# Optimization experiments

Measured on AMD Instinct MI355X. Metric: run time of the kernel, lower is better.

Reference implementation:

```python
import math
import jax, jax.numpy as jnp
import numpy as np

FIRE_THRESH = 0.85
_C = math.sqrt(2.0 / math.pi)

def _normalize(v, axis=-1, eps=1e-12):
    # matches torch F.normalize: v / max(||v||, eps)
    n = jnp.linalg.norm(v, axis=axis, keepdims=True)
    return v / jnp.maximum(n, eps)

def setup_inputs() -> dict:
    key = jax.random.key(0)
    k1, k2, k3 = jax.random.split(key, 3)
    B, T, D, N = 8, 4096, 1024, 512
    x = jax.random.normal(k1, (B, T, D), dtype=jnp.float32)
    buf = jax.random.normal(k2, (N, D), dtype=jnp.float32)
    depl = jax.random.uniform(k3, (N,), dtype=jnp.float32)
    mask = jnp.ones((N,), dtype=bool)
    ptr = 3  # static ring-buffer write position
    log_k = jnp.asarray(math.log(2.0), dtype=jnp.float32)
    logit_depl_rate = jnp.asarray(0.0, dtype=jnp.float32)
    logit_floor = jnp.asarray(math.log(0.1 / 0.9), dtype=jnp.float32)
    return {"x": x, "buf": buf, "depl": depl, "mask": mask, "ptr": ptr,
            "log_k": log_k, "logit_depl_rate": logit_depl_rate, "logit_floor": logit_floor}

def reference(x, buf, depl, mask, ptr, log_k, logit_depl_rate, logit_floor):
    # steady-state (_ready=True) forward of GELU244
    k_gate = jnp.clip(jnp.exp(log_k), 0.1, 8.0)
    depl_rate = 0.1 + 0.8 * jax.nn.sigmoid(logit_depl_rate)
    floor_val = 0.5 * jax.nn.sigmoid(logit_floor)
    # tanh-approx GELU
    y = 0.5 * x * (1.0 + jnp.tanh(_C * (x + 0.044715 * x ** 3)))  # [B,T,D]
    D = x.shape[-1]
    m_curr = jax.lax.stop_gradient(jnp.mean(y.reshape(-1, D), axis=0))  # [D]
    m_n = _normalize(m_curr, axis=0)  # unit vector [D]
    buf_n = _normalize(buf, axis=-1)  # [N,D]
    sims = jnp.where(mask, buf_n @ m_n, -1.0)  # [N]
    idx = jnp.argmax(sims)
    max_sim = sims[idx]
    depl_level = depl[idx]
    # .item() in torch => no grad through k_gate / depl_level here
    raw_gate = jnp.exp(-jax.lax.stop_gradient(k_gate) * (1.0 - jax.lax.stop_gradient(depl_level)))
    gate = floor_val + (1.0 - floor_val) * raw_gate
    output = y * gate
    # no_grad state update: deplete fired slot, write m_n at ring pointer
    factor = jnp.where(max_sim > FIRE_THRESH, jax.lax.stop_gradient(depl_rate), 1.0)
    new_depl = depl.at[idx].multiply(factor)
    new_buf = buf.at[ptr].set(m_n)
    new_depl = new_depl.at[ptr].set(1.0)
    new_mask = mask.at[ptr].set(True)
    return output, new_buf, new_depl, new_mask
```

## Files before the change

### kernel.cpp

```cpp
#include <hip/hip_runtime.h>
#include <math.h>

#define D_DIM    1024
#define D4       256
#define A_BLOCKS 1024
#define N_SLOTS  512
#define OUT_GRID 2048

#define GK1 0.07135481627f
#define GK2 1.59576912161f

typedef float f32x4 __attribute__((ext_vector_type(4)));

__device__ __forceinline__ float gelu_tanh(float x) {
    float t = x * __builtin_fmaf(GK1, x * x, GK2);
    float e = __expf(-t);
    return x * __builtin_amdgcn_rcpf(1.0f + e);
}

__global__ __launch_bounds__(256) void colsum_partial(
        const float* __restrict__ x, const float* __restrict__ buf,
        float* __restrict__ partial, float* __restrict__ out_buf,
        const int* __restrict__ ptr_p, int rows, int rows_per_block) {
    int t = threadIdx.x;
    int b = blockIdx.x;
    if (b < N_SLOTS && b != ptr_p[0])
        ((float4*)(out_buf + (size_t)b * D_DIM))[t] =
            ((const float4*)(buf + (size_t)b * D_DIM))[t];
    const float4* x4 = (const float4*)x;
    float4 acc = make_float4(0.f, 0.f, 0.f, 0.f);
    int r0 = b * rows_per_block;
    #pragma unroll 8
    for (int r = r0; r < r0 + rows_per_block; ++r) {
        float4 v = x4[(size_t)r * D4 + t];
        acc.x += gelu_tanh(v.x);
        acc.y += gelu_tanh(v.y);
        acc.z += gelu_tanh(v.z);
        acc.w += gelu_tanh(v.w);
    }
    ((float4*)partial)[(size_t)b * D4 + t] = acc;
}

__global__ __launch_bounds__(256) void reduce_cols(
        const float* __restrict__ partial, float* __restrict__ s_out) {
    __shared__ float red[8][32];
    int t  = threadIdx.x, b = blockIdx.x;
    int cl = t & 31, sl = t >> 5;
    int c  = b * 32 + cl;
    float s = 0.f;
    int p0 = sl * (A_BLOCKS / 8);
    #pragma unroll 4
    for (int p = p0; p < p0 + A_BLOCKS / 8; ++p)
        s += partial[(size_t)p * D_DIM + c];
    red[sl][cl] = s;
    __syncthreads();
    if (t < 32) {
        float tot = 0.f;
        #pragma unroll
        for (int i = 0; i < 8; ++i) tot += red[i][t];
        s_out[b * 32 + t] = tot;
    }
}

__global__ __launch_bounds__(256) void sims_dot(
        const float* __restrict__ buf, const float* __restrict__ s_vec,
        float* __restrict__ dotraw) {
    int n = blockIdx.x, t = threadIdx.x;
    int wid = t >> 6, lane = t & 63;
    float4 v = ((const float4*)(buf + (size_t)n * D_DIM))[t];
    float4 w = ((const float4*)s_vec)[t];
    float dot = v.x*w.x + v.y*w.y + v.z*w.z + v.w*w.w;
    float sq  = v.x*v.x + v.y*v.y + v.z*v.z + v.w*v.w;
    #pragma unroll
    for (int off = 32; off > 0; off >>= 1) {
        dot += __shfl_down(dot, off, 64);
        sq  += __shfl_down(sq,  off, 64);
    }
    __shared__ float rd[4], rs[4];
    if (lane == 0) { rd[wid] = dot; rs[wid] = sq; }
    __syncthreads();
    if (t == 0)
        dotraw[n] = (rd[0] + rd[1] + rd[2] + rd[3]) /
                    fmaxf(sqrtf(rs[0] + rs[1] + rs[2] + rs[3]), 1e-12f);
}

__global__ __launch_bounds__(256) void gate_stream_out(
        const float* __restrict__ x, const float* __restrict__ dotraw,
        const float* __restrict__ s_vec, const float* __restrict__ depl,
        const float* __restrict__ log_k, const float* __restrict__ logit_depl_rate,
        const float* __restrict__ logit_floor, const int* __restrict__ ptr_p,
        float* __restrict__ out, float* __restrict__ out_buf,
        float* __restrict__ out_depl, float* __restrict__ out_mask,
        int n4, float eps_s) {
    __shared__ float sval[256];
    __shared__ int   sidx[256];
    __shared__ float sgate;
    int t = threadIdx.x, b = blockIdx.x;

    {
        float a  = dotraw[t];
        float b2 = dotraw[t + 256];
        float v; int id;
        if (b2 > a) { v = b2; id = t + 256; } else { v = a; id = t; }
        sval[t] = v; sidx[t] = id;
        __syncthreads();
        for (int s = 128; s > 0; s >>= 1) {
            if (t < s) {
                float av = sval[t], bv = sval[t + s];
                int   ai = sidx[t], bi = sidx[t + s];
                if (bv > av || (bv == av && bi < ai)) { sval[t] = bv; sidx[t] = bi; }
            }
            __syncthreads();
        }
        if (t == 0) {
            int idx = sidx[0];
            float k_gate    = fminf(fmaxf(__expf(log_k[0]), 0.1f), 8.0f);
            float floor_val = 0.5f / (1.0f + __expf(-logit_floor[0]));
            float raw_gate  = __expf(-k_gate * (1.0f - depl[idx]));
            sgate = floor_val + (1.0f - floor_val) * raw_gate;
        }
        __syncthreads();
    }

    if (b == 0) {
        float4 w0 = ((const float4*)s_vec)[t];
        float sq = w0.x*w0.x + w0.y*w0.y + w0.z*w0.z + w0.w*w0.w;
        #pragma unroll
        for (int off = 32; off > 0; off >>= 1) sq += __shfl_down(sq, off, 64);
        __shared__ float rs2[4];
        __shared__ float ssnorm;
        int wid = t >> 6, lane = t & 63;
        if (lane == 0) rs2[wid] = sq;
        __syncthreads();
        if (t == 0)
            ssnorm = fmaxf(sqrtf(rs2[0] + rs2[1] + rs2[2] + rs2[3]), eps_s);
        __syncthreads();
        float snorm = ssnorm;
        int idx = sidx[0];
        int ptr = ptr_p[0];
        float max_sim   = sval[0] / snorm;
        float depl_rate = 0.1f + 0.8f / (1.0f + __expf(-logit_depl_rate[0]));
        float fac = (max_sim > 0.85f) ? depl_rate : 1.0f;
        #pragma unroll
        for (int j = t; j < N_SLOTS; j += 256) {
            float nd = depl[j] * (j == idx ? fac : 1.0f);
            if (j == ptr) nd = 1.0f;
            out_depl[j] = nd;
            out_mask[j] = 1.0f;
        }
        float inv = 1.0f / snorm;
        float4 sv = ((const float4*)s_vec)[t];
        float4 mn = make_float4(sv.x*inv, sv.y*inv, sv.z*inv, sv.w*inv);
        ((float4*)(out_buf + (size_t)ptr * D_DIM))[t] = mn;
    }

    float gate = sgate;
    const f32x4* x4 = (const f32x4*)x;
    f32x4* o4 = (f32x4*)out;
    #pragma unroll 4
    for (int i = b * 256 + t; i < n4; i += OUT_GRID * 256) {
        f32x4 v = x4[i];
        f32x4 r;
        r.x = gelu_tanh(v.x) * gate;
        r.y = gelu_tanh(v.y) * gate;
        r.z = gelu_tanh(v.z) * gate;
        r.w = gelu_tanh(v.w) * gate;
        __builtin_nontemporal_store(r, o4 + i);
    }
}

extern "C" void kernel_launch(void* const* d_in, const int* in_sizes, int n_in,
                              void* d_out, int out_size, void* d_ws, size_t ws_size,
                              hipStream_t stream) {
    const float* x     = (const float*)d_in[0];
    const float* buf   = (const float*)d_in[1];
    const float* depl  = (const float*)d_in[2];
    const int*   ptr_p = (const int*)d_in[4];
    const float* log_k = (const float*)d_in[5];
    const float* ldr   = (const float*)d_in[6];
    const float* lf    = (const float*)d_in[7];

    int xN   = in_sizes[0];
    int bufN = in_sizes[1];
    int rows = xN / D_DIM;

    float* out      = (float*)d_out;
    float* out_buf  = out + xN;
    float* out_depl = out_buf + bufN;
    float* out_mask = out_depl + N_SLOTS;

    float* ws      = (float*)d_ws;
    float* s_vec   = ws;
    float* dotraw  = ws + 1040;
    float* partial = ws + 2048;

    int rpb = rows / A_BLOCKS;
    float eps_s = 1e-12f * (float)rows;

    hipLaunchKernelGGL(colsum_partial, dim3(A_BLOCKS), dim3(256), 0, stream,
                       x, buf, partial, out_buf, ptr_p, rows, rpb);
    hipLaunchKernelGGL(reduce_cols, dim3(32), dim3(256), 0, stream,
                       partial, s_vec);
    hipLaunchKernelGGL(sims_dot, dim3(N_SLOTS), dim3(256), 0, stream,
                       buf, s_vec, dotraw);
    hipLaunchKernelGGL(gate_stream_out, dim3(OUT_GRID), dim3(256), 0, stream,
                       x, dotraw, s_vec, depl, log_k, ldr, lf, ptr_p,
                       out, out_buf, out_depl, out_mask, xN / 4, eps_s);
}
```

Baseline: 84.15 us.

## Stage GELU output as bf16 in workspace and stream gated output from it

The column-sum pass now also writes GELU(x) to a bf16 workspace buffer. The final gated-output pass reads this half-width buffer instead of re-reading fp32 x and recomputing GELU. This swaps a second fp32 read of x for a bf16 write plus read, and skips the GELU recompute. The output loses precision to bf16 rounding, and the path only runs when the workspace is large enough, falling back to the old path otherwise.

```diff
diff --git a/kernel.cpp b/kernel.cpp
--- a/kernel.cpp
+++ b/kernel.cpp
@@ -10,7 +10,9 @@
 #define GK1 0.07135481627f
 #define GK2 1.59576912161f
 
-typedef float f32x4 __attribute__((ext_vector_type(4)));
+typedef float          f32x4  __attribute__((ext_vector_type(4)));
+typedef unsigned short u16x4v __attribute__((ext_vector_type(4)));
+typedef unsigned short u16x8v __attribute__((ext_vector_type(8)));
 
 __device__ __forceinline__ float gelu_tanh(float x) {
     float t = x * __builtin_fmaf(GK1, x * x, GK2);
@@ -18,27 +20,128 @@
     return x * __builtin_amdgcn_rcpf(1.0f + e);
 }
 
-__global__ __launch_bounds__(256) void colsum_partial(
+__device__ __forceinline__ unsigned short f2bf(float f) {
+    unsigned u = __builtin_bit_cast(unsigned, f);
+    u += 0x7FFFu + ((u >> 16) & 1u);
+    return (unsigned short)(u >> 16);
+}
+__device__ __forceinline__ float bf2f(unsigned short h) {
+    return __builtin_bit_cast(float, ((unsigned)h) << 16);
+}
+
+__global__ __launch_bounds__(256) void colsum_stage_bf16(
         const float* __restrict__ x, const float* __restrict__ buf,
-        float* __restrict__ partial, float* __restrict__ out_buf,
-        const int* __restrict__ ptr_p, int rows, int rows_per_block) {
+        float* __restrict__ partial, unsigned short* __restrict__ y16,
+        float* __restrict__ out_buf, const int* __restrict__ ptr_p,
+        int rows, int rows_per_block) {
     int t = threadIdx.x;
     int b = blockIdx.x;
     if (b < N_SLOTS && b != ptr_p[0])
-        ((float4*)(out_buf + (size_t)b * D_DIM))[t] =
-            ((const float4*)(buf + (size_t)b * D_DIM))[t];
-    const float4* x4 = (const float4*)x;
-    float4 acc = make_float4(0.f, 0.f, 0.f, 0.f);
+        ((f32x4*)(out_buf + (size_t)b * D_DIM))[t] =
+            ((const f32x4*)(buf + (size_t)b * D_DIM))[t];
+    const f32x4* x4 = (const f32x4*)x;
+    u16x4v* y4 = (u16x4v*)y16;
+    f32x4 acc = {0.f, 0.f, 0.f, 0.f};
     int r0 = b * rows_per_block;
-    #pragma unroll 8
+    #pragma unroll 4
     for (int r = r0; r < r0 + rows_per_block; ++r) {
-        float4 v = x4[(size_t)r * D4 + t];
-        acc.x += gelu_tanh(v.x);
-        acc.y += gelu_tanh(v.y);
-        acc.z += gelu_tanh(v.z);
-        acc.w += gelu_tanh(v.w);
-    }
-    ((float4*)partial)[(size_t)b * D4 + t] = acc;
+        f32x4 v = x4[(size_t)r * D4 + t];
+        f32x4 y;
+        y.x = gelu_tanh(v.x);
+        y.y = gelu_tanh(v.y);
+        y.z = gelu_tanh(v.z);
+        y.w = gelu_tanh(v.w);
+        acc.x += y.x; acc.y += y.y; acc.z += y.z; acc.w += y.w;
+        u16x4v h = { f2bf(y.x), f2bf(y.y), f2bf(y.z), f2bf(y.w) };
+        y4[(size_t)r * D4 + t] = h;
+    }
+    ((f32x4*)partial)[(size_t)b * D4 + t] = acc;
+}
+
+__global__ __launch_bounds__(256) void gate_stream_bf16(
+        const unsigned short* __restrict__ y16, const float* __restrict__ dotraw,
+        const float* __restrict__ s_vec, const float* __restrict__ depl,
+        const float* __restrict__ log_k, const float* __restrict__ logit_depl_rate,
+        const float* __restrict__ logit_floor, const int* __restrict__ ptr_p,
+        float* __restrict__ out, float* __restrict__ out_buf,
+        float* __restrict__ out_depl, float* __restrict__ out_mask,
+        int n8, float eps_s) {
+    __shared__ float sval[256];
+    __shared__ int   sidx[256];
+    __shared__ float sgate;
+    int t = threadIdx.x, b = blockIdx.x;
+
+    {
+        float a  = dotraw[t];
+        float b2 = dotraw[t + 256];
+        float v; int id;
+        if (b2 > a) { v = b2; id = t + 256; } else { v = a; id = t; }
+        sval[t] = v; sidx[t] = id;
+        __syncthreads();
+        for (int s = 128; s > 0; s >>= 1) {
+            if (t < s) {
+                float av = sval[t], bv = sval[t + s];
+                int   ai = sidx[t], bi = sidx[t + s];
+                if (bv > av || (bv == av && bi < ai)) { sval[t] = bv; sidx[t] = bi; }
+            }
+            __syncthreads();
+        }
+        if (t == 0) {
+            int idx = sidx[0];
+            float k_gate    = fminf(fmaxf(__expf(log_k[0]), 0.1f), 8.0f);
+            float floor_val = 0.5f / (1.0f + __expf(-logit_floor[0]));
+            float raw_gate  = __expf(-k_gate * (1.0f - depl[idx]));
+            sgate = floor_val + (1.0f - floor_val) * raw_gate;
+        }
+        __syncthreads();
+    }
+
+    if (b == 0) {
+        f32x4 w0 = ((const f32x4*)s_vec)[t];
+        float sq = w0.x*w0.x + w0.y*w0.y + w0.z*w0.z + w0.w*w0.w;
+        #pragma unroll
+        for (int off = 32; off > 0; off >>= 1) sq += __shfl_down(sq, off, 64);
+        __shared__ float rs2[4];
+        __shared__ float ssnorm;
+        int wid = t >> 6, lane = t & 63;
+        if (lane == 0) rs2[wid] = sq;
+        __syncthreads();
+        if (t == 0)
+            ssnorm = fmaxf(sqrtf(rs2[0] + rs2[1] + rs2[2] + rs2[3]), eps_s);
+        __syncthreads();
+        float snorm = ssnorm;
+        int idx = sidx[0];
+        int ptr = ptr_p[0];
+        float max_sim   = sval[0] / snorm;
+        float depl_rate = 0.1f + 0.8f / (1.0f + __expf(-logit_depl_rate[0]));
+        float fac = (max_sim > 0.85f) ? depl_rate : 1.0f;
+        #pragma unroll
+        for (int j = t; j < N_SLOTS; j += 256) {
+            float nd = depl[j] * (j == idx ? fac : 1.0f);
+            if (j == ptr) nd = 1.0f;
+            out_depl[j] = nd;
+            out_mask[j] = 1.0f;
+        }
+        float inv = 1.0f / snorm;
+        f32x4 sv = ((const f32x4*)s_vec)[t];
+        f32x4 mn = { sv.x * inv, sv.y * inv, sv.z * inv, sv.w * inv };
+        ((f32x4*)(out_buf + (size_t)ptr * D_DIM))[t] = mn;
+    }
+
+    float gate = sgate;
+    const u16x8v* y8 = (const u16x8v*)y16;
+    f32x4* o4 = (f32x4*)out;
+    #pragma unroll 4
+    for (int j = b * 256 + t; j < n8; j += OUT_GRID * 256) {
+        u16x8v h = y8[j];
+        f32x4 r0, r1;
+        r0.x = bf2f(h[0]) * gate; r0.y = bf2f(h[1]) * gate;
+        r0.z = bf2f(h[2]) * gate; r0.w = bf2f(h[3]) * gate;
+        r1.x = bf2f(h[4]) * gate; r1.y = bf2f(h[5]) * gate;
+        r1.z = bf2f(h[6]) * gate; r1.w = bf2f(h[7]) * gate;
+        __builtin_nontemporal_store(r0, o4 + 2 * j);
+        __builtin_nontemporal_store(r1, o4 + 2 * j + 1);
+    }
 }
 
 __global__ __launch_bounds__(256) void reduce_cols(
@@ -67,8 +170,8 @@
         float* __restrict__ dotraw) {
     int n = blockIdx.x, t = threadIdx.x;
     int wid = t >> 6, lane = t & 63;
-    float4 v = ((const float4*)(buf + (size_t)n * D_DIM))[t];
-    float4 w = ((const float4*)s_vec)[t];
+    f32x4 v = ((const f32x4*)(buf + (size_t)n * D_DIM))[t];
+    f32x4 w = ((const f32x4*)s_vec)[t];
     float dot = v.x*w.x + v.y*w.y + v.z*w.z + v.w*w.w;
     float sq  = v.x*v.x + v.y*v.y + v.z*v.z + v.w*v.w;
     #pragma unroll
@@ -82,6 +185,28 @@
     if (t == 0)
         dotraw[n] = (rd[0] + rd[1] + rd[2] + rd[3]) /
                     fmaxf(sqrtf(rs[0] + rs[1] + rs[2] + rs[3]), 1e-12f);
+}
+
+__global__ __launch_bounds__(256) void colsum_partial(
+        const float* __restrict__ x, const float* __restrict__ buf,
+        float* __restrict__ partial, float* __restrict__ out_buf,
+        const int* __restrict__ ptr_p, int rows, int rows_per_block) {
+    int t = threadIdx.x, b = blockIdx.x;
+    if (b < N_SLOTS && b != ptr_p[0])
+        ((f32x4*)(out_buf + (size_t)b * D_DIM))[t] =
+            ((const f32x4*)(buf + (size_t)b * D_DIM))[t];
+    const f32x4* x4 = (const f32x4*)x;
+    f32x4 acc = {0.f, 0.f, 0.f, 0.f};
+    int r0 = b * rows_per_block;
+    #pragma unroll 8
+    for (int r = r0; r < r0 + rows_per_block; ++r) {
+        f32x4 v = x4[(size_t)r * D4 + t];
+        acc.x += gelu_tanh(v.x);
+        acc.y += gelu_tanh(v.y);
+        acc.z += gelu_tanh(v.z);
+        acc.w += gelu_tanh(v.w);
+    }
+    ((f32x4*)partial)[(size_t)b * D4 + t] = acc;
 }
 
 __global__ __launch_bounds__(256) void gate_stream_out(
@@ -96,7 +221,6 @@
     __shared__ int   sidx[256];
     __shared__ float sgate;
     int t = threadIdx.x, b = blockIdx.x;
-
     {
         float a  = dotraw[t];
         float b2 = dotraw[t + 256];
@@ -121,9 +245,8 @@
         }
         __syncthreads();
     }
-
     if (b == 0) {
-        float4 w0 = ((const float4*)s_vec)[t];
+        f32x4 w0 = ((const f32x4*)s_vec)[t];
         float sq = w0.x*w0.x + w0.y*w0.y + w0.z*w0.z + w0.w*w0.w;
         #pragma unroll
         for (int off = 32; off > 0; off >>= 1) sq += __shfl_down(sq, off, 64);
@@ -149,11 +272,10 @@
             out_mask[j] = 1.0f;
         }
         float inv = 1.0f / snorm;
-        float4 sv = ((const float4*)s_vec)[t];
-        float4 mn = make_float4(sv.x*inv, sv.y*inv, sv.z*inv, sv.w*inv);
-        ((float4*)(out_buf + (size_t)ptr * D_DIM))[t] = mn;
-    }
-
+        f32x4 sv = ((const f32x4*)s_vec)[t];
+        f32x4 mn = { sv.x * inv, sv.y * inv, sv.z * inv, sv.w * inv };
+        ((f32x4*)(out_buf + (size_t)ptr * D_DIM))[t] = mn;
+    }
     float gate = sgate;
     const f32x4* x4 = (const f32x4*)x;
     f32x4* o4 = (f32x4*)out;
@@ -193,17 +315,33 @@
     float* s_vec   = ws;
     float* dotraw  = ws + 1040;
     float* partial = ws + 2048;
+    unsigned short* y16 = (unsigned short*)(ws + 2048 + (size_t)A_BLOCKS * D_DIM);
 
     int rpb = rows / A_BLOCKS;
     float eps_s = 1e-12f * (float)rows;
 
-    hipLaunchKernelGGL(colsum_partial, dim3(A_BLOCKS), dim3(256), 0, stream,
-                       x, buf, partial, out_buf, ptr_p, rows, rpb);
-    hipLaunchKernelGGL(reduce_cols, dim3(32), dim3(256), 0, stream,
-                       partial, s_vec);
-    hipLaunchKernelGGL(sims_dot, dim3(N_SLOTS), dim3(256), 0, stream,
-                       buf, s_vec, dotraw);
-    hipLaunchKernelGGL(gate_stream_out, dim3(OUT_GRID), dim3(256), 0, stream,
-                       x, dotraw, s_vec, depl, log_k, ldr, lf, ptr_p,
-                       out, out_buf, out_depl, out_mask, xN / 4, eps_s);
-}
+    size_t need = ((size_t)(2048 + A_BLOCKS * D_DIM)) * sizeof(float)
+                + (size_t)xN * sizeof(unsigned short);
+
+    if (ws_size >= need) {
+        hipLaunchKernelGGL(colsum_stage_bf16, dim3(A_BLOCKS), dim3(256), 0, stream,
+                           x, buf, partial, y16, out_buf, ptr_p, rows, rpb);
+        hipLaunchKernelGGL(reduce_cols, dim3(32), dim3(256), 0, stream,
+                           partial, s_vec);
+        hipLaunchKernelGGL(sims_dot, dim3(N_SLOTS), dim3(256), 0, stream,
+                           buf, s_vec, dotraw);
+        hipLaunchKernelGGL(gate_stream_bf16, dim3(OUT_GRID), dim3(256), 0, stream,
+                           y16, dotraw, s_vec, depl, log_k, ldr, lf, ptr_p,
+                           out, out_buf, out_depl, out_mask, xN / 8, eps_s);
+    } else {
+        hipLaunchKernelGGL(colsum_partial, dim3(A_BLOCKS), dim3(256), 0, stream,
+                           x, buf, partial, out_buf, ptr_p, rows, rpb);
+        hipLaunchKernelGGL(reduce_cols, dim3(32), dim3(256), 0, stream,
+                           partial, s_vec);
+        hipLaunchKernelGGL(sims_dot, dim3(N_SLOTS), dim3(256), 0, stream,
+                           buf, s_vec, dotraw);
+        hipLaunchKernelGGL(gate_stream_out, dim3(OUT_GRID), dim3(256), 0, stream,
+                           x, dotraw, s_vec, depl, log_k, ldr, lf, ptr_p,
+                           out, out_buf, out_depl, out_mask, xN / 4, eps_s);
+    }
+}
```

Measured after the change: 111.3 us. +32.3%, slower.

## Speculate gate from sampled column mean, fuse output with colsum, fix up on mismatch

Applied to the files above, without the earlier changes.

Estimates the mean vector from a 1/8 row sample, picks the best-matching slot and gate from that estimate, then does one fused pass over x that writes gated outputs and accumulates the exact column sums. Afterward it computes the exact argmax and gate, and rescales the output in a fixup kernel only when the exact gate differs from the estimate. This removes the second full read of x in the common case. It adds a small sampling pass and more launches, and costs a full extra read-write of the output whenever the speculation is wrong.

```diff
diff --git a/kernel.cpp b/kernel.cpp
--- a/kernel.cpp
+++ b/kernel.cpp
@@ -4,8 +4,9 @@
 #define D_DIM    1024
 #define D4       256
 #define A_BLOCKS 1024
+#define S_BLOCKS 256
 #define N_SLOTS  512
-#define OUT_GRID 2048
+#define FIX_GRID 2048
 
 #define GK1 0.07135481627f
 #define GK2 1.59576912161f
@@ -18,57 +19,58 @@
     return x * __builtin_amdgcn_rcpf(1.0f + e);
 }
 
-__global__ __launch_bounds__(256) void colsum_partial(
-        const float* __restrict__ x, const float* __restrict__ buf,
-        float* __restrict__ partial, float* __restrict__ out_buf,
-        const int* __restrict__ ptr_p, int rows, int rows_per_block) {
-    int t = threadIdx.x;
-    int b = blockIdx.x;
-    if (b < N_SLOTS && b != ptr_p[0])
-        ((float4*)(out_buf + (size_t)b * D_DIM))[t] =
-            ((const float4*)(buf + (size_t)b * D_DIM))[t];
-    const float4* x4 = (const float4*)x;
-    float4 acc = make_float4(0.f, 0.f, 0.f, 0.f);
-    int r0 = b * rows_per_block;
-    #pragma unroll 8
-    for (int r = r0; r < r0 + rows_per_block; ++r) {
-        float4 v = x4[(size_t)r * D4 + t];
+__device__ __forceinline__ float gate_from(float depl_idx, float log_k, float lf) {
+    float k_gate    = fminf(fmaxf(__expf(log_k), 0.1f), 8.0f);
+    float floor_val = 0.5f / (1.0f + __expf(-lf));
+    float raw_gate  = __expf(-k_gate * (1.0f - depl_idx));
+    return floor_val + (1.0f - floor_val) * raw_gate;
+}
+
+__global__ __launch_bounds__(256) void samp_partial(
+        const float* __restrict__ x, float* __restrict__ samp) {
+    int t = threadIdx.x, b = blockIdx.x;
+    const f32x4* x4 = (const f32x4*)x;
+    f32x4 acc = {0.f, 0.f, 0.f, 0.f};
+    #pragma unroll 4
+    for (int j = 0; j < 16; ++j) {
+        int r = 128 * b + 8 * j;
+        f32x4 v = x4[(size_t)r * D4 + t];
         acc.x += gelu_tanh(v.x);
         acc.y += gelu_tanh(v.y);
         acc.z += gelu_tanh(v.z);
         acc.w += gelu_tanh(v.w);
     }
-    ((float4*)partial)[(size_t)b * D4 + t] = acc;
-}
-
-__global__ __launch_bounds__(256) void reduce_cols(
-        const float* __restrict__ partial, float* __restrict__ s_out) {
+    ((f32x4*)samp)[(size_t)b * D4 + t] = acc;
+}
+
+__global__ __launch_bounds__(256) void samp_reduce(
+        const float* __restrict__ samp, float* __restrict__ s_est) {
     __shared__ float red[8][32];
-    int t  = threadIdx.x, b = blockIdx.x;
+    int t = threadIdx.x, b = blockIdx.x;
     int cl = t & 31, sl = t >> 5;
     int c  = b * 32 + cl;
     float s = 0.f;
-    int p0 = sl * (A_BLOCKS / 8);
-    #pragma unroll 4
-    for (int p = p0; p < p0 + A_BLOCKS / 8; ++p)
-        s += partial[(size_t)p * D_DIM + c];
+    #pragma unroll 4
+    for (int p = sl * 32; p < sl * 32 + 32; ++p)
+        s += samp[(size_t)p * D_DIM + c];
     red[sl][cl] = s;
     __syncthreads();
     if (t < 32) {
         float tot = 0.f;
         #pragma unroll
         for (int i = 0; i < 8; ++i) tot += red[i][t];
-        s_out[b * 32 + t] = tot;
-    }
-}
-
-__global__ __launch_bounds__(256) void sims_dot(
-        const float* __restrict__ buf, const float* __restrict__ s_vec,
-        float* __restrict__ dotraw) {
+        s_est[b * 32 + t] = tot;
+    }
+}
+
+__global__ __launch_bounds__(256) void sims_est_copy(
+        const float* __restrict__ buf, const float* __restrict__ s_est,
+        float* __restrict__ dotraw_est, float* __restrict__ out_buf,
+        const int* __restrict__ ptr_p) {
     int n = blockIdx.x, t = threadIdx.x;
     int wid = t >> 6, lane = t & 63;
-    float4 v = ((const float4*)(buf + (size_t)n * D_DIM))[t];
-    float4 w = ((const float4*)s_vec)[t];
+    f32x4 v = ((const f32x4*)(buf + (size_t)n * D_DIM))[t];
+    f32x4 w = ((const f32x4*)s_est)[t];
     float dot = v.x*w.x + v.y*w.y + v.z*w.z + v.w*w.w;
     float sq  = v.x*v.x + v.y*v.y + v.z*v.z + v.w*v.w;
     #pragma unroll
@@ -80,26 +82,25 @@
     if (lane == 0) { rd[wid] = dot; rs[wid] = sq; }
     __syncthreads();
     if (t == 0)
-        dotraw[n] = (rd[0] + rd[1] + rd[2] + rd[3]) /
-                    fmaxf(sqrtf(rs[0] + rs[1] + rs[2] + rs[3]), 1e-12f);
-}
-
-__global__ __launch_bounds__(256) void gate_stream_out(
-        const float* __restrict__ x, const float* __restrict__ dotraw,
-        const float* __restrict__ s_vec, const float* __restrict__ depl,
-        const float* __restrict__ log_k, const float* __restrict__ logit_depl_rate,
-        const float* __restrict__ logit_floor, const int* __restrict__ ptr_p,
-        float* __restrict__ out, float* __restrict__ out_buf,
-        float* __restrict__ out_depl, float* __restrict__ out_mask,
-        int n4, float eps_s) {
+        dotraw_est[n] = (rd[0] + rd[1] + rd[2] + rd[3]) /
+                        fmaxf(sqrtf(rs[0] + rs[1] + rs[2] + rs[3]), 1e-12f);
+    if (n != ptr_p[0])
+        ((f32x4*)(out_buf + (size_t)n * D_DIM))[t] = v;
+}
+
+__global__ __launch_bounds__(256) void big_pass(
+        const float* __restrict__ x, const float* __restrict__ dotraw_est,
+        const float* __restrict__ depl, const float* __restrict__ log_k,
+        const float* __restrict__ lf, float* __restrict__ out,
+        float* __restrict__ partial, float* __restrict__ gate_est_out,
+        int rows_per_block) {
     __shared__ float sval[256];
     __shared__ int   sidx[256];
     __shared__ float sgate;
     int t = threadIdx.x, b = blockIdx.x;
-
     {
-        float a  = dotraw[t];
-        float b2 = dotraw[t + 256];
+        float a  = dotraw_est[t];
+        float b2 = dotraw_est[t + 256];
         float v; int id;
         if (b2 > a) { v = b2; id = t + 256; } else { v = a; id = t; }
         sval[t] = v; sidx[t] = id;
@@ -113,58 +114,141 @@
             __syncthreads();
         }
         if (t == 0) {
-            int idx = sidx[0];
-            float k_gate    = fminf(fmaxf(__expf(log_k[0]), 0.1f), 8.0f);
-            float floor_val = 0.5f / (1.0f + __expf(-logit_floor[0]));
-            float raw_gate  = __expf(-k_gate * (1.0f - depl[idx]));
-            sgate = floor_val + (1.0f - floor_val) * raw_gate;
+            sgate = gate_from(depl[sidx[0]], log_k[0], lf[0]);
+            if (b == 0) gate_est_out[0] = sgate;
         }
         __syncthreads();
     }
-
-    if (b == 0) {
-        float4 w0 = ((const float4*)s_vec)[t];
-        float sq = w0.x*w0.x + w0.y*w0.y + w0.z*w0.z + w0.w*w0.w;
-        #pragma unroll
-        for (int off = 32; off > 0; off >>= 1) sq += __shfl_down(sq, off, 64);
-        __shared__ float rs2[4];
-        __shared__ float ssnorm;
-        int wid = t >> 6, lane = t & 63;
-        if (lane == 0) rs2[wid] = sq;
-        __syncthreads();
-        if (t == 0)
-            ssnorm = fmaxf(sqrtf(rs2[0] + rs2[1] + rs2[2] + rs2[3]), eps_s);
-        __syncthreads();
-        float snorm = ssnorm;
-        int idx = sidx[0];
-        int ptr = ptr_p[0];
-        float max_sim   = sval[0] / snorm;
-        float depl_rate = 0.1f + 0.8f / (1.0f + __expf(-logit_depl_rate[0]));
-        float fac = (max_sim > 0.85f) ? depl_rate : 1.0f;
-        #pragma unroll
-        for (int j = t; j < N_SLOTS; j += 256) {
-            float nd = depl[j] * (j == idx ? fac : 1.0f);
-            if (j == ptr) nd = 1.0f;
-            out_depl[j] = nd;
-            out_mask[j] = 1.0f;
-        }
-        float inv = 1.0f / snorm;
-        float4 sv = ((const float4*)s_vec)[t];
-        float4 mn = make_float4(sv.x*inv, sv.y*inv, sv.z*inv, sv.w*inv);
-        ((float4*)(out_buf + (size_t)ptr * D_DIM))[t] = mn;
-    }
-
     float gate = sgate;
     const f32x4* x4 = (const f32x4*)x;
     f32x4* o4 = (f32x4*)out;
-    #pragma unroll 4
-    for (int i = b * 256 + t; i < n4; i += OUT_GRID * 256) {
-        f32x4 v = x4[i];
-        f32x4 r;
-        r.x = gelu_tanh(v.x) * gate;
-        r.y = gelu_tanh(v.y) * gate;
-        r.z = gelu_tanh(v.z) * gate;
-        r.w = gelu_tanh(v.w) * gate;
+    f32x4 acc = {0.f, 0.f, 0.f, 0.f};
+    int r0 = b * rows_per_block;
+    #pragma unroll 4
+    for (int r = r0; r < r0 + rows_per_block; ++r) {
+        f32x4 v = x4[(size_t)r * D4 + t];
+        f32x4 y;
+        y.x = gelu_tanh(v.x);
+        y.y = gelu_tanh(v.y);
+        y.z = gelu_tanh(v.z);
+        y.w = gelu_tanh(v.w);
+        acc.x += y.x; acc.y += y.y; acc.z += y.z; acc.w += y.w;
+        f32x4 o = { y.x * gate, y.y * gate, y.z * gate, y.w * gate };
+        __builtin_nontemporal_store(o, o4 + (size_t)r * D4 + t);
+    }
+    ((f32x4*)partial)[(size_t)b * D4 + t] = acc;
+}
+
+__global__ __launch_bounds__(256) void reduce_cols(
+        const float* __restrict__ partial, float* __restrict__ s_out) {
+    __shared__ float red[8][32];
+    int t = threadIdx.x, b = blockIdx.x;
+    int cl = t & 31, sl = t >> 5;
+    int c  = b * 32 + cl;
+    float s = 0.f;
+    int p0 = sl * (A_BLOCKS / 8);
+    #pragma unroll 4
+    for (int p = p0; p < p0 + A_BLOCKS / 8; ++p)
+        s += partial[(size_t)p * D_DIM + c];
+    red[sl][cl] = s;
+    __syncthreads();
+    if (t < 32) {
+        float tot = 0.f;
+        #pragma unroll
+        for (int i = 0; i < 8; ++i) tot += red[i][t];
+        s_out[b * 32 + t] = tot;
+    }
+}
+
+__global__ __launch_bounds__(256) void sims_dot(
+        const float* __restrict__ buf, const float* __restrict__ s_vec,
+        float* __restrict__ dotraw) {
+    int n = blockIdx.x, t = threadIdx.x;
+    int wid = t >> 6, lane = t & 63;
+    f32x4 v = ((const f32x4*)(buf + (size_t)n * D_DIM))[t];
+    f32x4 w = ((const f32x4*)s_vec)[t];
+    float dot = v.x*w.x + v.y*w.y + v.z*w.z + v.w*w.w;
+    float sq  = v.x*v.x + v.y*v.y + v.z*v.z + v.w*v.w;
+    #pragma unroll
+    for (int off = 32; off > 0; off >>= 1) {
+        dot += __shfl_down(dot, off, 64);
+        sq  += __shfl_down(sq,  off, 64);
+    }
+    __shared__ float rd[4], rs[4];
+    if (lane == 0) { rd[wid] = dot; rs[wid] = sq; }
+    __syncthreads();
+    if (t == 0)
+        dotraw[n] = (rd[0] + rd[1] + rd[2] + rd[3]) /
+                    fmaxf(sqrtf(rs[0] + rs[1] + rs[2] + rs[3]), 1e-12f);
+}
+
+__global__ __launch_bounds__(512) void gate_state_cmp(
+        const float* __restrict__ dotraw, const float* __restrict__ s_vec,
+        const float* __restrict__ depl, const float* __restrict__ log_k,
+        const float* __restrict__ logit_depl_rate, const float* __restrict__ lf,
+        const int* __restrict__ ptr_p, const float* __restrict__ gate_est_p,
+        float* __restrict__ ratio_out, float* __restrict__ out_depl,
+        float* __restrict__ out_mask, float* __restrict__ out_buf,
+        float eps_s) {
+    __shared__ float sval[512];
+    __shared__ int   sidx[512];
+    int t = threadIdx.x;
+    sval[t] = dotraw[t];
+    sidx[t] = t;
+    __syncthreads();
+    for (int s = 256; s > 0; s >>= 1) {
+        if (t < s) {
+            float a = sval[t], b = sval[t + s];
+            int ia = sidx[t], ib = sidx[t + s];
+            if (b > a || (b == a && ib < ia)) { sval[t] = b; sidx[t] = ib; }
+        }
+        __syncthreads();
+    }
+    __shared__ float rs2[8];
+    float e0 = s_vec[t], e1 = s_vec[t + 512];
+    float sq = e0 * e0 + e1 * e1;
+    #pragma unroll
+    for (int off = 32; off > 0; off >>= 1) sq += __shfl_down(sq, off, 64);
+    int wid = t >> 6, lane = t & 63;
+    if (lane == 0) rs2[wid] = sq;
+    __syncthreads();
+    __shared__ float sfac, ssnorm;
+    __shared__ int sIdx;
+    if (t == 0) {
+        float tot = 0.f;
+        #pragma unroll
+        for (int i = 0; i < 8; ++i) tot += rs2[i];
+        float snorm = fmaxf(sqrtf(tot), eps_s);
+        ssnorm = snorm;
+        int idx = sidx[0];
+        float max_sim = sval[0] / snorm;
+        float gate_exact = gate_from(depl[idx], log_k[0], lf[0]);
+        ratio_out[0] = gate_exact / gate_est_p[0];
+        float depl_rate = 0.1f + 0.8f / (1.0f + __expf(-logit_depl_rate[0]));
+        sfac = (max_sim > 0.85f) ? depl_rate : 1.0f;
+        sIdx = idx;
+    }
+    __syncthreads();
+    int ptr = ptr_p[0];
+    float nd = depl[t] * (t == sIdx ? sfac : 1.0f);
+    if (t == ptr) nd = 1.0f;
+    out_depl[t] = nd;
+    out_mask[t] = 1.0f;
+    float inv = 1.0f / ssnorm;
+    out_buf[(size_t)ptr * D_DIM + t]       = s_vec[t]       * inv;
+    out_buf[(size_t)ptr * D_DIM + t + 512] = s_vec[t + 512] * inv;
+}
+
+__global__ __launch_bounds__(256) void fixup_scale(
+        float* __restrict__ out, const float* __restrict__ ratio_p, int n4) {
+    float ratio = ratio_p[0];
+    if (ratio == 1.0f) return;
+    int t = threadIdx.x, b = blockIdx.x;
+    f32x4* o4 = (f32x4*)out;
+    #pragma unroll 4
+    for (int i = b * 256 + t; i < n4; i += FIX_GRID * 256) {
+        f32x4 v = o4[i];
+        f32x4 r = { v.x * ratio, v.y * ratio, v.z * ratio, v.w * ratio };
         __builtin_nontemporal_store(r, o4 + i);
     }
 }
@@ -189,21 +273,35 @@
     float* out_depl = out_buf + bufN;
     float* out_mask = out_depl + N_SLOTS;
 
-    float* ws      = (float*)d_ws;
-    float* s_vec   = ws;
-    float* dotraw  = ws + 1040;
-    float* partial = ws + 2048;
+    float* ws         = (float*)d_ws;
+    float* s_vec      = ws;
+    float* dotraw     = ws + 1024;
+    float* s_est      = ws + 1536;
+    float* dotraw_est = ws + 2560;
+    float* gate_est_w = ws + 3072;
+    float* ratio_w    = ws + 3088;
+    float* samp       = ws + 4096;
+    float* partial    = samp + (size_t)S_BLOCKS * D_DIM;
 
     int rpb = rows / A_BLOCKS;
     float eps_s = 1e-12f * (float)rows;
 
-    hipLaunchKernelGGL(colsum_partial, dim3(A_BLOCKS), dim3(256), 0, stream,
-                       x, buf, partial, out_buf, ptr_p, rows, rpb);
+    hipLaunchKernelGGL(samp_partial, dim3(S_BLOCKS), dim3(256), 0, stream,
+                       x, samp);
+    hipLaunchKernelGGL(samp_reduce, dim3(32), dim3(256), 0, stream,
+                       samp, s_est);
+    hipLaunchKernelGGL(sims_est_copy, dim3(N_SLOTS), dim3(256), 0, stream,
+                       buf, s_est, dotraw_est, out_buf, ptr_p);
+    hipLaunchKernelGGL(big_pass, dim3(A_BLOCKS), dim3(256), 0, stream,
+                       x, dotraw_est, depl, log_k, lf, out, partial,
+                       gate_est_w, rpb);
     hipLaunchKernelGGL(reduce_cols, dim3(32), dim3(256), 0, stream,
                        partial, s_vec);
     hipLaunchKernelGGL(sims_dot, dim3(N_SLOTS), dim3(256), 0, stream,
                        buf, s_vec, dotraw);
-    hipLaunchKernelGGL(gate_stream_out, dim3(OUT_GRID), dim3(256), 0, stream,
-                       x, dotraw, s_vec, depl, log_k, ldr, lf, ptr_p,
-                       out, out_buf, out_depl, out_mask, xN / 4, eps_s);
-}
+    hipLaunchKernelGGL(gate_state_cmp, dim3(1), dim3(512), 0, stream,
+                       dotraw, s_vec, depl, log_k, ldr, lf, ptr_p,
+                       gate_est_w, ratio_w, out_depl, out_mask, out_buf, eps_s);
+    hipLaunchKernelGGL(fixup_scale, dim3(FIX_GRID), dim3(256), 0, stream,
+                       out, ratio_w, xN / 4);
+}
```

Measured after the change: 80.61 us, median of 2. 4.2% less time.
